# Optimization experiments

Hardware: AMD Instinct MI355X
Metric: run time of the kernel (lower is better)

## Reference

```python
import jax, jax.numpy as jnp
import numpy as np

S = 7  # output_size
B, C, HF, WF = 8, 256, 160, 160
N = 128
IMG = 640


def setup_inputs() -> dict:
    key = jax.random.key(0)
    k1, k2, k3, k4 = jax.random.split(key, 4)
    feature_map = jax.random.normal(k1, (B, C, HF, WF), jnp.float32)
    # boxes in image-pixel coordinates (the module divides by image_size itself)
    pts = jax.random.uniform(k2, (B, N, 2, 2), jnp.float32, 0.0, float(IMG))
    lo = jnp.min(pts, axis=2)  # (x1, y1)
    hi = jnp.max(pts, axis=2)  # (x2, y2)
    bboxes = jnp.concatenate([lo, hi], axis=-1)  # [B, N, 4]
    proj_w = jax.random.normal(k3, (C, C), jnp.float32) * (1.0 / np.sqrt(C))
    proj_b = jax.random.normal(k4, (C,), jnp.float32) * 0.01
    return {"feature_map": feature_map, "bboxes": bboxes,
            "proj_w": proj_w, "proj_b": proj_b,
            "image_h": IMG, "image_w": IMG}


def _forward(feature_map, bboxes, proj_w, proj_b, image_h, image_w):
    Bb, Cc, Hf, Wf = feature_map.shape
    # 1x1 conv projection
    f = jnp.einsum('bchw,oc->bohw', feature_map, proj_w) + proj_b[None, :, None, None]
    # scale boxes from image coords to feature coords, then integer clip (as in torch code)
    sx = float(Wf) / float(image_w)
    sy = float(Hf) / float(image_h)
    x1 = jnp.clip(jnp.floor(bboxes[..., 0] * sx).astype(jnp.int32), 0, Wf - 1)
    y1 = jnp.clip(jnp.floor(bboxes[..., 1] * sy).astype(jnp.int32), 0, Hf - 1)
    x2 = jnp.clip(jnp.floor(bboxes[..., 2] * sx).astype(jnp.int32), x1 + 1, Wf)
    y2 = jnp.clip(jnp.floor(bboxes[..., 3] * sy).astype(jnp.int32), y1 + 1, Hf)
    Lx = x2 - x1  # [B, N], >= 1 by construction
    Ly = y2 - y1
    i = jnp.arange(S, dtype=jnp.int32)
    # adaptive_avg_pool2d bin edges: start=floor(i*L/S), end=ceil((i+1)*L/S)
    rs = y1[..., None] + (i * Ly[..., None]) // S            # [B, N, S]
    re = y1[..., None] + ((i + 1) * Ly[..., None] + S - 1) // S
    cs = x1[..., None] + (i * Lx[..., None]) // S
    ce = x1[..., None] + ((i + 1) * Lx[..., None] + S - 1) // S
    # summed-area table (zero-padded): I[b,c,y,x] = sum of f[b,c,:y,:x]
    I = jnp.cumsum(jnp.cumsum(f, axis=2), axis=3)
    I = jnp.pad(I, ((0, 0), (0, 0), (1, 0), (1, 0)))

    def per_batch(Ib, rs_b, re_b, cs_b, ce_b):
        # Ib: [C, Hf+1, Wf+1]; index arrays: [N, S]
        tl = Ib[:, rs_b[:, :, None], cs_b[:, None, :]]
        tr = Ib[:, rs_b[:, :, None], ce_b[:, None, :]]
        bl = Ib[:, re_b[:, :, None], cs_b[:, None, :]]
        br = Ib[:, re_b[:, :, None], ce_b[:, None, :]]
        return br - tr - bl + tl  # [C, N, S, S]

    sums = jax.vmap(per_batch)(I, rs, re, cs, ce)  # [B, C, N, S, S]
    counts = ((re - rs)[..., :, None] * (ce - cs)[..., None, :]).astype(f.dtype)  # [B, N, S, S]
    region_features = jnp.transpose(sums, (0, 2, 1, 3, 4)) / counts[:, :, None, :, :]
    # area in raw bbox units, as in the original code
    area_ratios = (bboxes[..., 2] - bboxes[..., 0]) * (bboxes[..., 3] - bboxes[..., 1])
    return region_features, area_ratios


def reference(feature_map, bboxes, proj_w, proj_b, image_h, image_w):
    return _forward(feature_map, bboxes, proj_w, proj_b, image_h, image_w)
```

## Files before the change

kernel.cpp:

```cpp
#include <hip/hip_runtime.h>
#include <hip/hip_bf16.h>

#define BB 8
#define NN 128
#define CC 256
#define HFD 160
#define WFD 160
#define SS 7
#define REGION_OUT_ELEMS (8*128*256*49)

typedef short short8 __attribute__((ext_vector_type(8)));
typedef float f32x4  __attribute__((ext_vector_type(4)));

__global__ __launch_bounds__(256) void k0_convert_w(const float* __restrict__ W,
                                                    __hip_bfloat16* __restrict__ Wb) {
    int o = blockIdx.x;
    int c = threadIdx.x;
    Wb[o * CC + c] = __float2bfloat16(W[o * CC + c]);
}

__global__ __launch_bounds__(256) void k1_rowsum_transpose(const float* __restrict__ fm,
                                                           float* __restrict__ R) {
    int bid = blockIdx.x;
    int cq  = bid & 3;
    int bh  = bid >> 2;
    int h   = bh % HFD;
    int b   = bh / HFD;
    int c0  = cq * 64;
    int t   = threadIdx.x;

    __shared__ float tile[64][161];
    __shared__ float segsum[64][5];

    #pragma unroll
    for (int it = 0; it < 10; ++it) {
        int vid = it * 256 + t;
        int c_l = vid / 40;
        int wq  = vid - c_l * 40;
        f32x4 v = __builtin_nontemporal_load(
            (const f32x4*)(fm + (((size_t)(b * CC + c0 + c_l)) * HFD + h) * WFD + wq * 4));
        tile[c_l][wq * 4 + 0] = v.x;
        tile[c_l][wq * 4 + 1] = v.y;
        tile[c_l][wq * 4 + 2] = v.z;
        tile[c_l][wq * 4 + 3] = v.w;
    }
    __syncthreads();

    int seg = t >> 6;
    int row = t & 63;
    {
        float s = 0.f;
        int w0 = seg * 40;
        #pragma unroll 8
        for (int k = 0; k < 40; ++k) {
            s += tile[row][w0 + k];
            tile[row][w0 + k] = s;
        }
        segsum[row][seg] = s;
    }
    __syncthreads();
    if (t < 64) {
        float a0 = segsum[t][0];
        float a1 = a0 + segsum[t][1];
        float a2 = a1 + segsum[t][2];
        segsum[t][1] = a0;
        segsum[t][2] = a1;
        segsum[t][3] = a2;
    }
    __syncthreads();
    if (seg > 0) {
        float off = segsum[row][seg];
        int w0 = seg * 40;
        #pragma unroll 8
        for (int k = 0; k < 40; ++k) tile[row][w0 + k] += off;
    }
    __syncthreads();

    size_t obase = (((size_t)b * HFD + h) * WFD) * CC + c0;
    #pragma unroll
    for (int it = 0; it < 10; ++it) {
        int vid = it * 256 + t;
        int w   = vid >> 4;
        int cg  = vid & 15;
        float4 o;
        o.x = tile[cg * 4 + 0][w];
        o.y = tile[cg * 4 + 1][w];
        o.z = tile[cg * 4 + 2][w];
        o.w = tile[cg * 4 + 3][w];
        *(float4*)(R + obase + (size_t)w * CC + cg * 4) = o;
    }
}

__global__ __launch_bounds__(256) void k2_colsum(float* __restrict__ I) {
    int w = blockIdx.x % WFD;
    int b = blockIdx.x / WFD;
    int c = threadIdx.x;
    float* p = I + (((size_t)b * HFD) * WFD + w) * CC + c;
    const size_t stride = (size_t)WFD * CC;
    float s = 0.f;
    #pragma unroll 16
    for (int h = 0; h < HFD; ++h) {
        float v = p[(size_t)h * stride];
        s += v;
        p[(size_t)h * stride] = s;
    }
}

#define PB_STRIDE 264

__global__ __launch_bounds__(512) void k3_gather_gemm(
        const float* __restrict__ I, const __hip_bfloat16* __restrict__ Wb,
        const float* __restrict__ bias, const float* __restrict__ bboxes,
        const int* __restrict__ ih_p, const int* __restrict__ iw_p,
        float* __restrict__ out) {
    int bn = blockIdx.x;
    int b  = bn >> 7;
    int t  = threadIdx.x;
    const int lane = t & 63;
    const int wv   = t >> 6;

    __shared__ __hip_bfloat16 Pb[64 * PB_STRIDE];

    float bx1 = bboxes[bn * 4 + 0];
    float by1 = bboxes[bn * 4 + 1];
    float bx2 = bboxes[bn * 4 + 2];
    float by2 = bboxes[bn * 4 + 3];
    float sx = (float)WFD / (float)iw_p[0];
    float sy = (float)HFD / (float)ih_p[0];

    int x1 = min(max((int)floorf(bx1 * sx), 0), WFD - 1);
    int y1 = min(max((int)floorf(by1 * sy), 0), HFD - 1);
    int x2 = min(max((int)floorf(bx2 * sx), x1 + 1), WFD);
    int y2 = min(max((int)floorf(by2 * sy), y1 + 1), HFD);
    int Lx = x2 - x1, Ly = y2 - y1;

    {
        const float* Ibl = I + (size_t)b * HFD * WFD * CC + 4 * lane;
        unsigned short* pbs = (unsigned short*)Pb;

        #pragma unroll
        for (int k = 0; k < 7; ++k) {
            int cell = wv + 8 * k;
            int cc_  = min(cell, 48);
            int i_ = cc_ / SS, j_ = cc_ % SS;

            int rs_ = y1 + (i_ * Ly) / SS;
            int re_ = y1 + ((i_ + 1) * Ly + SS - 1) / SS;
            int cs_ = x1 + (j_ * Lx) / SS;
            int ce_ = x1 + ((j_ + 1) * Lx + SS - 1) / SS;

            int r1 = re_ - 1;
            int r0 = max(rs_ - 1, 0);
            int c1 = ce_ - 1;
            int c0 = max(cs_ - 1, 0);
            float rm = (rs_ > 0) ? 1.f : 0.f;
            float cm = (cs_ > 0) ? 1.f : 0.f;

            f32x4 br = *(const f32x4*)(Ibl + ((size_t)(r1 * WFD + c1)) * CC);
            f32x4 tr = *(const f32x4*)(Ibl + ((size_t)(r0 * WFD + c1)) * CC);
            f32x4 bl = *(const f32x4*)(Ibl + ((size_t)(r1 * WFD + c0)) * CC);
            f32x4 tl = *(const f32x4*)(Ibl + ((size_t)(r0 * WFD + c0)) * CC);

            f32x4 s = (br - tr * rm) - (bl - tl * rm) * cm;
            float inv = 1.f / ((float)(re_ - rs_) * (float)(ce_ - cs_));

            ushort4 pk;
            {
                __hip_bfloat16 h0 = __float2bfloat16(s.x * inv);
                __hip_bfloat16 h1 = __float2bfloat16(s.y * inv);
                __hip_bfloat16 h2 = __float2bfloat16(s.z * inv);
                __hip_bfloat16 h3 = __float2bfloat16(s.w * inv);
                pk.x = *(unsigned short*)&h0;
                pk.y = *(unsigned short*)&h1;
                pk.z = *(unsigned short*)&h2;
                pk.w = *(unsigned short*)&h3;
            }
            *(ushort4*)(pbs + cell * PB_STRIDE + 4 * lane) = pk;
        }
    }
    __syncthreads();

    {
        const int ln   = lane & 15;
        const int quad = lane >> 4;
        const int ob0  = wv * 32;

        f32x4 z = {0.f, 0.f, 0.f, 0.f};
        f32x4 acc[2][4];
        #pragma unroll
        for (int mt = 0; mt < 2; ++mt)
            #pragma unroll
            for (int nt = 0; nt < 4; ++nt) acc[mt][nt] = z;

        const short* A = (const short*)Wb;
        #pragma unroll
        for (int k0 = 0; k0 < CC; k0 += 32) {
            short8 a[2], bf[4];
            #pragma unroll
            for (int mt = 0; mt < 2; ++mt)
                a[mt] = *(const short8*)(A + (ob0 + mt * 16 + ln) * CC + k0 + quad * 8);
            #pragma unroll
            for (int nt = 0; nt < 4; ++nt)
                bf[nt] = *(const short8*)((const short*)Pb + (nt * 16 + ln) * PB_STRIDE + k0 + quad * 8);
            #pragma unroll
            for (int mt = 0; mt < 2; ++mt)
                #pragma unroll
                for (int nt = 0; nt < 4; ++nt)
                    acc[mt][nt] = __builtin_amdgcn_mfma_f32_16x16x32_bf16(a[mt], bf[nt], acc[mt][nt], 0, 0, 0);
        }

        size_t obase = (size_t)bn * CC * 49;
        #pragma unroll
        for (int mt = 0; mt < 2; ++mt) {
            f32x4 bv = *(const f32x4*)(bias + ob0 + mt * 16 + quad * 4);
            #pragma unroll
            for (int nt = 0; nt < 4; ++nt) {
                int cell = nt * 16 + ln;
                if (cell < 49) {
                    #pragma unroll
                    for (int reg = 0; reg < 4; ++reg) {
                        int o = ob0 + mt * 16 + quad * 4 + reg;
                        __builtin_nontemporal_store(acc[mt][nt][reg] + bv[reg],
                                                    &out[obase + (size_t)o * 49 + cell]);
                    }
                }
            }
        }
    }

    if (t == 0) {
        __builtin_nontemporal_store((bx2 - bx1) * (by2 - by1), &out[REGION_OUT_ELEMS + bn]);
    }
}

extern "C" void kernel_launch(void* const* d_in, const int* in_sizes, int n_in,
                              void* d_out, int out_size, void* d_ws, size_t ws_size,
                              hipStream_t stream) {
    const float* fm     = (const float*)d_in[0];
    const float* bboxes = (const float*)d_in[1];
    const float* W      = (const float*)d_in[2];
    const float* bias   = (const float*)d_in[3];
    const int*   ih     = (const int*)d_in[4];
    const int*   iw     = (const int*)d_in[5];
    float* out = (float*)d_out;

    __hip_bfloat16* Wb = (__hip_bfloat16*)d_ws;
    float* I = (float*)((char*)d_ws + (size_t)CC * CC * 2 + 256);
    I = (float*)(((uintptr_t)I + 1023) & ~(uintptr_t)1023);

    k0_convert_w<<<CC, 256, 0, stream>>>(W, Wb);
    k1_rowsum_transpose<<<BB * HFD * 4, 256, 0, stream>>>(fm, I);
    k2_colsum<<<BB * WFD, 256, 0, stream>>>(I);
    k3_gather_gemm<<<BB * NN, 512, 0, stream>>>(I, Wb, bias, bboxes, ih, iw, out);
}
```

Before: 427.5 us.

## Stage GEMM output through LDS for coalesced stores, remap blocks, rebalance gather

The block index is remapped so consecutive blocks come from different batches, the gather work is split into six contiguous cells per wave with one extra cell on wave 0, and the epilogue now writes results into shared memory in two halves before streaming them out as coalesced 16-byte nontemporal stores. The old epilogue issued scattered 4-byte stores with a stride of 49 floats. The new one adds extra barriers and LDS traffic, and the unchanged LDS buffer must be large enough to hold a 128x49 float staging tile.

```diff
diff --git a/kernel.cpp b/kernel.cpp
--- a/kernel.cpp
+++ b/kernel.cpp
@@ -113,13 +113,15 @@
         const float* __restrict__ bias, const float* __restrict__ bboxes,
         const int* __restrict__ ih_p, const int* __restrict__ iw_p,
         float* __restrict__ out) {
-    int bn = blockIdx.x;
-    int b  = bn >> 7;
-    int t  = threadIdx.x;
+    int bid = blockIdx.x;
+    int bn  = ((bid & 7) << 7) | (bid >> 3);
+    int b   = bn >> 7;
+    int t   = threadIdx.x;
     const int lane = t & 63;
     const int wv   = t >> 6;
 
-    __shared__ __hip_bfloat16 Pb[64 * PB_STRIDE];
+    __shared__ __align__(16) __hip_bfloat16 Pb[64 * PB_STRIDE];
+    float* stage = (float*)Pb;
 
     float bx1 = bboxes[bn * 4 + 0];
     float by1 = bboxes[bn * 4 + 1];
@@ -138,60 +140,59 @@
         const float* Ibl = I + (size_t)b * HFD * WFD * CC + 4 * lane;
         unsigned short* pbs = (unsigned short*)Pb;
 
+#define GATHER_CELL(cellv)                                                       \
+        {                                                                        \
+            int cell = (cellv);                                                  \
+            int i_ = cell / SS, j_ = cell % SS;                                  \
+            int rs_ = y1 + (i_ * Ly) / SS;                                       \
+            int re_ = y1 + ((i_ + 1) * Ly + SS - 1) / SS;                        \
+            int cs_ = x1 + (j_ * Lx) / SS;                                       \
+            int ce_ = x1 + ((j_ + 1) * Lx + SS - 1) / SS;                        \
+            int r1 = re_ - 1;                                                    \
+            int r0 = max(rs_ - 1, 0);                                            \
+            int c1 = ce_ - 1;                                                    \
+            int c0 = max(cs_ - 1, 0);                                            \
+            float rm = (rs_ > 0) ? 1.f : 0.f;                                    \
+            float cm = (cs_ > 0) ? 1.f : 0.f;                                    \
+            f32x4 br = *(const f32x4*)(Ibl + ((size_t)(r1 * WFD + c1)) * CC);    \
+            f32x4 tr = *(const f32x4*)(Ibl + ((size_t)(r0 * WFD + c1)) * CC);    \
+            f32x4 bl = *(const f32x4*)(Ibl + ((size_t)(r1 * WFD + c0)) * CC);    \
+            f32x4 tl = *(const f32x4*)(Ibl + ((size_t)(r0 * WFD + c0)) * CC);    \
+            f32x4 s = (br - tr * rm) - (bl - tl * rm) * cm;                      \
+            float inv = 1.f / ((float)(re_ - rs_) * (float)(ce_ - cs_));         \
+            ushort4 pk;                                                          \
+            {                                                                    \
+                __hip_bfloat16 h0 = __float2bfloat16(s.x * inv);                 \
+                __hip_bfloat16 h1 = __float2bfloat16(s.y * inv);                 \
+                __hip_bfloat16 h2 = __float2bfloat16(s.z * inv);                 \
+                __hip_bfloat16 h3 = __float2bfloat16(s.w * inv);                 \
+                pk.x = *(unsigned short*)&h0;                                    \
+                pk.y = *(unsigned short*)&h1;                                    \
+                pk.z = *(unsigned short*)&h2;                                    \
+                pk.w = *(unsigned short*)&h3;                                    \
+            }                                                                    \
+            *(ushort4*)(pbs + cell * PB_STRIDE + 4 * lane) = pk;                 \
+        }
+
         #pragma unroll
-        for (int k = 0; k < 7; ++k) {
-            int cell = wv + 8 * k;
-            int cc_  = min(cell, 48);
-            int i_ = cc_ / SS, j_ = cc_ % SS;
-
-            int rs_ = y1 + (i_ * Ly) / SS;
-            int re_ = y1 + ((i_ + 1) * Ly + SS - 1) / SS;
-            int cs_ = x1 + (j_ * Lx) / SS;
-            int ce_ = x1 + ((j_ + 1) * Lx + SS - 1) / SS;
-
-            int r1 = re_ - 1;
-            int r0 = max(rs_ - 1, 0);
-            int c1 = ce_ - 1;
-            int c0 = max(cs_ - 1, 0);
-            float rm = (rs_ > 0) ? 1.f : 0.f;
-            float cm = (cs_ > 0) ? 1.f : 0.f;
-
-            f32x4 br = *(const f32x4*)(Ibl + ((size_t)(r1 * WFD + c1)) * CC);
-            f32x4 tr = *(const f32x4*)(Ibl + ((size_t)(r0 * WFD + c1)) * CC);
-            f32x4 bl = *(const f32x4*)(Ibl + ((size_t)(r1 * WFD + c0)) * CC);
-            f32x4 tl = *(const f32x4*)(Ibl + ((size_t)(r0 * WFD + c0)) * CC);
-
-            f32x4 s = (br - tr * rm) - (bl - tl * rm) * cm;
-            float inv = 1.f / ((float)(re_ - rs_) * (float)(ce_ - cs_));
-
-            ushort4 pk;
-            {
-                __hip_bfloat16 h0 = __float2bfloat16(s.x * inv);
-                __hip_bfloat16 h1 = __float2bfloat16(s.y * inv);
-                __hip_bfloat16 h2 = __float2bfloat16(s.z * inv);
-                __hip_bfloat16 h3 = __float2bfloat16(s.w * inv);
-                pk.x = *(unsigned short*)&h0;
-                pk.y = *(unsigned short*)&h1;
-                pk.z = *(unsigned short*)&h2;
-                pk.w = *(unsigned short*)&h3;
-            }
-            *(ushort4*)(pbs + cell * PB_STRIDE + 4 * lane) = pk;
-        }
-    }
-    __syncthreads();
+        for (int k = 0; k < 6; ++k) GATHER_CELL(wv * 6 + k);
+        if (wv == 0) GATHER_CELL(48);
+#undef GATHER_CELL
+    }
+    __syncthreads();
+
+    const int ln   = lane & 15;
+    const int quad = lane >> 4;
+    const int ob0  = wv * 32;
+
+    f32x4 z = {0.f, 0.f, 0.f, 0.f};
+    f32x4 acc[2][4];
+    #pragma unroll
+    for (int mt = 0; mt < 2; ++mt)
+        #pragma unroll
+        for (int nt = 0; nt < 4; ++nt) acc[mt][nt] = z;
 
     {
-        const int ln   = lane & 15;
-        const int quad = lane >> 4;
-        const int ob0  = wv * 32;
-
-        f32x4 z = {0.f, 0.f, 0.f, 0.f};
-        f32x4 acc[2][4];
-        #pragma unroll
-        for (int mt = 0; mt < 2; ++mt)
-            #pragma unroll
-            for (int nt = 0; nt < 4; ++nt) acc[mt][nt] = z;
-
         const short* A = (const short*)Wb;
         #pragma unroll
         for (int k0 = 0; k0 < CC; k0 += 32) {
@@ -208,23 +209,35 @@
                 for (int nt = 0; nt < 4; ++nt)
                     acc[mt][nt] = __builtin_amdgcn_mfma_f32_16x16x32_bf16(a[mt], bf[nt], acc[mt][nt], 0, 0, 0);
         }
-
-        size_t obase = (size_t)bn * CC * 49;
-        #pragma unroll
-        for (int mt = 0; mt < 2; ++mt) {
-            f32x4 bv = *(const f32x4*)(bias + ob0 + mt * 16 + quad * 4);
-            #pragma unroll
-            for (int nt = 0; nt < 4; ++nt) {
-                int cell = nt * 16 + ln;
-                if (cell < 49) {
-                    #pragma unroll
-                    for (int reg = 0; reg < 4; ++reg) {
-                        int o = ob0 + mt * 16 + quad * 4 + reg;
-                        __builtin_nontemporal_store(acc[mt][nt][reg] + bv[reg],
-                                                    &out[obase + (size_t)o * 49 + cell]);
+    }
+
+    size_t obase = (size_t)bn * CC * 49;
+    #pragma unroll
+    for (int half = 0; half < 2; ++half) {
+        __syncthreads();
+        if ((wv >> 2) == half) {
+            int ob0l = (wv & 3) * 32;
+            #pragma unroll
+            for (int mt = 0; mt < 2; ++mt) {
+                f32x4 bv = *(const f32x4*)(bias + ob0 + mt * 16 + quad * 4);
+                #pragma unroll
+                for (int nt = 0; nt < 4; ++nt) {
+                    int cell = nt * 16 + ln;
+                    if (cell < 49) {
+                        #pragma unroll
+                        for (int reg = 0; reg < 4; ++reg) {
+                            int ol = ob0l + mt * 16 + quad * 4 + reg;
+                            stage[ol * 49 + cell] = acc[mt][nt][reg] + bv[reg];
+                        }
                     }
                 }
             }
+        }
+        __syncthreads();
+        const f32x4* sv = (const f32x4*)stage;
+        float* gbase = out + obase + (size_t)half * (128 * 49);
+        for (int i = t; i < (128 * 49) / 4; i += 512) {
+            __builtin_nontemporal_store(sv[i], (f32x4*)(gbase + 4 * i));
         }
     }
 
```

Result: faster. 411.0 us (-3.9%).
